# Kernel optimization log

Measured on AMD Instinct MI355X. Metric: run time of the kernel, lower is better.

Reference implementation:

```python
import jax, jax.numpy as jnp
import numpy as np

N, E, H = 20000, 320000, 2
F_IN, D, D_OUT, NMID = 17, 64, 32, 18
SLOPE, EPS = 0.2, 1e-5


def _gat(x, Wl, bl, Wr, br, att, bias, src, dst, n, h, c):
    # PyG GATv2Conv, heads=h, concat=False (mean over heads)
    xl = (x @ Wl + bl).reshape(n, h, c)   # source transform
    xr = (x @ Wr + br).reshape(n, h, c)   # target transform
    e = jax.nn.leaky_relu(xl[src] + xr[dst], SLOPE)        # [E,h,c]
    logit = jnp.sum(e * att, axis=-1)                       # [E,h]
    m = jax.ops.segment_max(logit, dst, num_segments=n)    # per-dst softmax
    a = jnp.exp(logit - m[dst])
    s = jax.ops.segment_sum(a, dst, num_segments=n)
    alpha = a / s[dst]
    out = jax.ops.segment_sum(alpha[..., None] * xl[src], dst, num_segments=n)
    return out.mean(axis=1) + bias


def _bn(x, g, b):
    # BatchNorm1d in training mode (batch statistics, biased variance)
    mu = x.mean(axis=0)
    var = jnp.mean((x - mu) ** 2, axis=0)
    return g * (x - mu) * jax.lax.rsqrt(var + EPS) + b


def setup_inputs() -> dict:
    key = jax.random.key(0)
    ks = iter(jax.random.split(key, 64))
    r = lambda *s: jax.random.normal(next(ks), s, jnp.float32) * 0.1
    return dict(
        x=jax.random.normal(next(ks), (N, F_IN), jnp.float32),
        src=jax.random.randint(next(ks), (E,), 0, N),
        dst=jax.random.randint(next(ks), (E,), 0, N),
        W0l=r(F_IN, H * D), b0l=r(H * D), W0r=r(F_IN, H * D), b0r=r(H * D),
        att0=r(H, D), bias0=r(D), g0=jnp.ones((D,), jnp.float32), be0=jnp.zeros((D,), jnp.float32),
        Wml=r(NMID, D, H * D), bml=r(NMID, H * D), Wmr=r(NMID, D, H * D), bmr=r(NMID, H * D),
        attm=r(NMID, H, D), biasm=r(NMID, D), gm=jnp.ones((NMID, D), jnp.float32), bem=jnp.zeros((NMID, D), jnp.float32),
        WLl=r(D, H * D_OUT), bLl=r(H * D_OUT), WLr=r(D, H * D_OUT), bLr=r(H * D_OUT),
        attL=r(H, D_OUT), biasL=r(D_OUT), gL=jnp.ones((D_OUT,), jnp.float32), beL=jnp.zeros((D_OUT,), jnp.float32),
        Wimp=r(D_OUT, 1), bimp=r(1), Wpol=r(D_OUT, 1), bpol=r(1),
    )


def reference(x, src, dst, W0l, b0l, W0r, b0r, att0, bias0, g0, be0,
              Wml, bml, Wmr, bmr, attm, biasm, gm, bem,
              WLl, bLl, WLr, bLr, attL, biasL, gL, beL,
              Wimp, bimp, Wpol, bpol):
    n = x.shape[0]
    loop = jnp.arange(n, dtype=src.dtype)  # add_self_loops=True (PyG default)
    s = jnp.concatenate([src, loop])
    d = jnp.concatenate([dst, loop])
    h = jax.nn.relu(_bn(_gat(x, W0l, b0l, W0r, b0r, att0, bias0, s, d, n, H, D), g0, be0))
    for i in range(NMID):
        h = h + jax.nn.relu(_bn(_gat(h, Wml[i], bml[i], Wmr[i], bmr[i], attm[i], biasm[i], s, d, n, H, D), gm[i], bem[i]))
    h = jax.nn.relu(_bn(_gat(h, WLl, bLl, WLr, bLr, attL, biasL, s, d, n, H, D_OUT), gL, beL))
    return (h @ Wimp + bimp, jax.nn.sigmoid(h @ Wpol + bpol))
```

## Files before the change

### kernel.cpp

```cpp
#include <hip/hip_runtime.h>
#include <hip/hip_fp16.h>
#include <math.h>

#define NN 20000
#define NE 320000
#define ET (NE + NN)
#define FIN 17
#define DD 64
#define DOUTC 32
#define NMIDL 18
#define SLOPE 0.2f
#define BN_EPS 1e-5f

typedef unsigned short ushortT;
typedef unsigned int uintT;

__device__ inline ushortT f2h(float x) { return __half_as_ushort(__float2half(x)); }
__device__ inline float2 h2unpack(uintT u) {
    __half2 h2 = *(__half2*)&u;
    return __half22float2(h2);
}


__global__ void k_init(int* __restrict__ deg, float* __restrict__ part) {
    int i = blockIdx.x * blockDim.x + threadIdx.x;
    if (i < NN) deg[i] = 1;
    if (i < 2 * 64 * 128) part[i] = 0.f;
}

__global__ void k_hist(const int* __restrict__ dst, int* __restrict__ deg) {
    int i = blockIdx.x * blockDim.x + threadIdx.x;
    if (i < NE) atomicAdd(&deg[dst[i]], 1);
}

__global__ __launch_bounds__(1024) void k_scan(const int* __restrict__ deg,
                                               int* __restrict__ row_ptr,
                                               int* __restrict__ cursor) {
    __shared__ int sarr[1024];
    int t = threadIdx.x;
    const int CH = 20;
    int base = t * CH;
    int sum = 0;
    for (int j = 0; j < CH; ++j) {
        int idx = base + j;
        if (idx < NN) sum += deg[idx];
    }
    sarr[t] = sum;
    __syncthreads();
    for (int off = 1; off < 1024; off <<= 1) {
        int v = (t >= off) ? sarr[t - off] : 0;
        __syncthreads();
        sarr[t] += v;
        __syncthreads();
    }
    int run = sarr[t] - sum;
    for (int j = 0; j < CH; ++j) {
        int idx = base + j;
        if (idx < NN) {
            row_ptr[idx] = run;
            cursor[idx] = run;
            run += deg[idx];
        }
    }
    if (t == 0) row_ptr[NN] = ET;
}

__global__ void k_scatter(const int* __restrict__ src, const int* __restrict__ dst,
                          int* __restrict__ cursor, int* __restrict__ edge_src) {
    int i = blockIdx.x * blockDim.x + threadIdx.x;
    if (i < NE) {
        int d = dst[i];
        int pos = atomicAdd(&cursor[d], 1);
        edge_src[pos] = src[i];
    } else if (i < ET) {
        int v = i - NE;
        int pos = atomicAdd(&cursor[v], 1);
        edge_src[pos] = v;
    }
}


template<int DIN, int DCOLS>
__global__ __launch_bounds__(256) void k_gemm3(const float* __restrict__ hin,
                                               const float* __restrict__ Wl, const float* __restrict__ bl,
                                               const float* __restrict__ Wr, const float* __restrict__ br,
                                               ushortT* __restrict__ xl, ushortT* __restrict__ xr) {
    constexpr int CG = (2 * DCOLS) / 64;
    constexpr int NSETS = 4 / CG;
    constexpr int NPB = NSETS * 4;
    int wave = __builtin_amdgcn_readfirstlane(threadIdx.x >> 6);
    int lane = threadIdx.x & 63;
    int cg = wave % CG;
    int nset = wave / CG;
    int col = cg * 64 + lane;
    bool isl = col < DCOLS;
    const float* W = isl ? Wl : Wr;
    ushortT* xo = isl ? xl : xr;
    int cw = col & (DCOLS - 1);
    float wreg[DIN];
    #pragma unroll
    for (int k = 0; k < DIN; ++k) wreg[k] = W[k * DCOLS + cw];
    float bias = (isl ? bl : br)[cw];

    for (int n0 = blockIdx.x * NPB + nset * 4; n0 < NN; n0 += gridDim.x * NPB) {
        const float* h0 = hin + (size_t)n0 * DIN;
        float a0 = 0.f, a1 = 0.f, a2 = 0.f, a3 = 0.f;
        #pragma unroll
        for (int k = 0; k < DIN; ++k) {
            float wk = wreg[k];
            a0 = fmaf(h0[k],           wk, a0);
            a1 = fmaf(h0[DIN + k],     wk, a1);
            a2 = fmaf(h0[2 * DIN + k], wk, a2);
            a3 = fmaf(h0[3 * DIN + k], wk, a3);
        }
        xo[(size_t)(n0 + 0) * DCOLS + cw] = f2h(a0 + bias);
        xo[(size_t)(n0 + 1) * DCOLS + cw] = f2h(a1 + bias);
        xo[(size_t)(n0 + 2) * DCOLS + cw] = f2h(a2 + bias);
        xo[(size_t)(n0 + 3) * DCOLS + cw] = f2h(a3 + bias);
    }
}


template<int DCOLS>
__global__ __launch_bounds__(256) void k_gemm_fused(
        const float* __restrict__ g, const float* __restrict__ part,
        float* __restrict__ partZero,
        const float* __restrict__ gam, const float* __restrict__ bet,
        int addres, float* __restrict__ hbuf,
        const float* __restrict__ Wl, const float* __restrict__ bl,
        const float* __restrict__ Wr, const float* __restrict__ br,
        ushortT* __restrict__ xl, ushortT* __restrict__ xr) {
    constexpr int DIN = 64;
    constexpr int CG = (2 * DCOLS) / 64;
    constexpr int NSETS = 4 / CG;
    constexpr int NPB = NSETS * 4;
    __shared__ float sscale[64], sshift[64];
    __shared__ float hlds[NPB][64];
    int tid = threadIdx.x;

    if (blockIdx.x == 0) {
        for (int i = tid; i < 64 * 128; i += 256) partZero[i] = 0.f;
    }
    {
        int c = tid & 63, half = tid >> 6;
        if (half < 2) {
            float ssum = 0.f;
            for (int s = 0; s < 64; ++s) ssum += part[s * 128 + half * 64 + c];
            hlds[half][c] = ssum;
        }
    }
    __syncthreads();
    if (tid < 64) {
        float mu  = hlds[0][tid] * (1.f / NN);
        float var = hlds[1][tid] * (1.f / NN) - mu * mu;
        float sc  = gam[tid] * rsqrtf(var + BN_EPS);
        sscale[tid] = sc;
        sshift[tid] = bet[tid] - sc * mu;
    }

    int wave = __builtin_amdgcn_readfirstlane(tid >> 6);
    int lane = tid & 63;
    int cg = wave % CG;
    int nset = wave / CG;
    int col = cg * 64 + lane;
    bool isl = col < DCOLS;
    const float* W = isl ? Wl : Wr;
    ushortT* xo = isl ? xl : xr;
    int cw = col & (DCOLS - 1);
    float wreg[DIN];
    #pragma unroll
    for (int k = 0; k < DIN; ++k) wreg[k] = W[k * DCOLS + cw];
    float bias = (isl ? bl : br)[cw];

    for (int n0 = blockIdx.x * NPB; n0 < NN; n0 += gridDim.x * NPB) {
        __syncthreads();
        #pragma unroll
        for (int v = 0; v < (NPB * 64) / 256; ++v) {
            int idx = tid + v * 256;
            int nl = idx >> 6, c = idx & 63;
            int node = n0 + nl;
            float gv = g[(size_t)node * 64 + c];
            float hv = fmaxf(fmaf(sscale[c], gv, sshift[c]), 0.f);
            if (addres) hv += hbuf[(size_t)node * 64 + c];
            hlds[nl][c] = hv;
            hbuf[(size_t)node * 64 + c] = hv;
        }
        __syncthreads();
        int nb = nset * 4;
        float a0 = 0.f, a1 = 0.f, a2 = 0.f, a3 = 0.f;
        #pragma unroll
        for (int k4 = 0; k4 < 16; ++k4) {
            float4 h0 = *(const float4*)&hlds[nb + 0][k4 * 4];
            float4 h1 = *(const float4*)&hlds[nb + 1][k4 * 4];
            float4 h2 = *(const float4*)&hlds[nb + 2][k4 * 4];
            float4 h3 = *(const float4*)&hlds[nb + 3][k4 * 4];
            a0 = fmaf(h0.x, wreg[k4*4+0], a0); a0 = fmaf(h0.y, wreg[k4*4+1], a0);
            a0 = fmaf(h0.z, wreg[k4*4+2], a0); a0 = fmaf(h0.w, wreg[k4*4+3], a0);
            a1 = fmaf(h1.x, wreg[k4*4+0], a1); a1 = fmaf(h1.y, wreg[k4*4+1], a1);
            a1 = fmaf(h1.z, wreg[k4*4+2], a1); a1 = fmaf(h1.w, wreg[k4*4+3], a1);
            a2 = fmaf(h2.x, wreg[k4*4+0], a2); a2 = fmaf(h2.y, wreg[k4*4+1], a2);
            a2 = fmaf(h2.z, wreg[k4*4+2], a2); a2 = fmaf(h2.w, wreg[k4*4+3], a2);
            a3 = fmaf(h3.x, wreg[k4*4+0], a3); a3 = fmaf(h3.y, wreg[k4*4+1], a3);
            a3 = fmaf(h3.z, wreg[k4*4+2], a3); a3 = fmaf(h3.w, wreg[k4*4+3], a3);
        }
        int nbase = n0 + nb;
        xo[(size_t)(nbase + 0) * DCOLS + cw] = f2h(a0 + bias);
        xo[(size_t)(nbase + 1) * DCOLS + cw] = f2h(a1 + bias);
        xo[(size_t)(nbase + 2) * DCOLS + cw] = f2h(a2 + bias);
        xo[(size_t)(nbase + 3) * DCOLS + cw] = f2h(a3 + bias);
    }
}


template<int CPL>
__global__ __launch_bounds__(256) void k_edge_stat(const ushortT* __restrict__ xl,
                                                   const ushortT* __restrict__ xr,
                                                   const float* __restrict__ att,
                                                   const float* __restrict__ bias,
                                                   const int* __restrict__ row_ptr,
                                                   const int* __restrict__ edge_src,
                                                   float* __restrict__ g,
                                                   float* __restrict__ partial) {
    constexpr int HC = CPL * 32;
    constexpr int RS = 2 * HC;
    int lane = threadIdx.x & 63;
    int node = blockIdx.x * 4 + (threadIdx.x >> 6);
    if (node >= NN) return;
    int co = lane * CPL;
    float2 xrv, attc;
    if (CPL == 2) {
        uintT ur = ((const uintT*)xr)[(size_t)node * (RS / 2) + lane];
        xrv = h2unpack(ur);
        attc = *(const float2*)&att[co];
    } else {
        xrv.x = __half2float(__ushort_as_half(xr[(size_t)node * RS + co]));
        xrv.y = 0.f;
        attc.x = att[co];
        attc.y = 0.f;
    }
    int beg = row_ptr[node], end = row_ptr[node + 1];
    float m = -1e30f, s = 0.f;
    float2 o = {0.f, 0.f};

    for (int cb = beg; cb < end; cb += 64) {
        int idx = cb + lane;
        int eload = edge_src[idx < end ? idx : end - 1];
        int cnt = min(64, end - cb);
        for (int b = 0; b < cnt; b += 8) {
            int nb = min(8, cnt - b);
            float p[8]; float2 xv[8];
            #pragma unroll
            for (int j = 0; j < 8; ++j) {
                int u = __shfl(eload, b + (j < nb ? j : 0));
                float2 v;
                if (CPL == 2) {
                    uintT uu = ((const uintT*)xl)[(size_t)u * (RS / 2) + lane];
                    v = h2unpack(uu);
                } else {
                    v.x = __half2float(__ushort_as_half(xl[(size_t)u * RS + co]));
                    v.y = 0.f;
                }
                xv[j] = v;
                float tx = v.x + xrv.x, ty = v.y + xrv.y;
                tx = tx > 0.f ? tx : SLOPE * tx;
                ty = ty > 0.f ? ty : SLOPE * ty;
                float pp = tx * attc.x + ty * attc.y;
                #pragma unroll
                for (int msk = 16; msk; msk >>= 1) pp += __shfl_xor(pp, msk);
                p[j] = (j < nb) ? pp : -1e30f;
            }
            float nm = fmaxf(fmaxf(fmaxf(p[0], p[1]), fmaxf(p[2], p[3])),
                             fmaxf(fmaxf(p[4], p[5]), fmaxf(p[6], p[7])));
            if (nm > m + 8.f) {
                float sc = __expf(m - nm);
                s *= sc; o.x *= sc; o.y *= sc;
                m = nm;
            }
            float w0 = __expf(p[0] - m), w1 = __expf(p[1] - m);
            float w2 = __expf(p[2] - m), w3 = __expf(p[3] - m);
            float w4 = __expf(p[4] - m), w5 = __expf(p[5] - m);
            float w6 = __expf(p[6] - m), w7 = __expf(p[7] - m);
            s += ((w0 + w1) + (w2 + w3)) + ((w4 + w5) + (w6 + w7));
            o.x += ((w0 * xv[0].x + w1 * xv[1].x) + (w2 * xv[2].x + w3 * xv[3].x))
                 + ((w4 * xv[4].x + w5 * xv[5].x) + (w6 * xv[6].x + w7 * xv[7].x));
            o.y += ((w0 * xv[0].y + w1 * xv[1].y) + (w2 * xv[2].y + w3 * xv[3].y))
                 + ((w4 * xv[4].y + w5 * xv[5].y) + (w6 * xv[6].y + w7 * xv[7].y));
        }
    }
    float inv = 1.f / s;
    float rx = o.x * inv, ry = o.y * inv;
    float ox = __shfl_xor(rx, 32);
    float oy = __shfl_xor(ry, 32);
    if (lane < 32) {
        float* ps = &partial[(size_t)(node & 63) * 128];
        if (CPL == 2) {
            float2 bv = *(const float2*)&bias[co];
            float2 outv = { 0.5f * (rx + ox) + bv.x, 0.5f * (ry + oy) + bv.y };
            *(float2*)&g[(size_t)node * HC + co] = outv;
            atomicAdd(&ps[co],     outv.x);
            atomicAdd(&ps[co + 1], outv.y);
            atomicAdd(&ps[64 + co],     outv.x * outv.x);
            atomicAdd(&ps[64 + co + 1], outv.y * outv.y);
        } else {
            float ov = 0.5f * (rx + ox) + bias[co];
            g[(size_t)node * HC + co] = ov;
            atomicAdd(&ps[co], ov);
            atomicAdd(&ps[64 + co], ov * ov);
        }
    }
}


__global__ __launch_bounds__(256) void k_headf(const float* __restrict__ g,
                                               const float* __restrict__ part,
                                               const float* __restrict__ gL, const float* __restrict__ beL,
                                               const float* __restrict__ Wimp, const float* __restrict__ bimp,
                                               const float* __restrict__ Wpol, const float* __restrict__ bpol,
                                               float* __restrict__ out) {
    __shared__ float tmp[2][32];
    __shared__ float sscale[32], sshift[32], swi[32], swp[32];
    int tid = threadIdx.x;
    if (tid < 64) {
        int c = tid & 31, half = tid >> 5;
        float ssum = 0.f;
        for (int s = 0; s < 64; ++s) ssum += part[s * 128 + half * 64 + c];
        tmp[half][c] = ssum;
    }
    __syncthreads();
    if (tid < 32) {
        float mu  = tmp[0][tid] * (1.f / NN);
        float var = tmp[1][tid] * (1.f / NN) - mu * mu;
        float sc  = gL[tid] * rsqrtf(var + BN_EPS);
        sscale[tid] = sc;
        sshift[tid] = beL[tid] - sc * mu;
        swi[tid] = Wimp[tid];
        swp[tid] = Wpol[tid];
    }
    __syncthreads();
    int n = blockIdx.x * 256 + tid;
    if (n >= NN) return;
    float a1 = bimp[0], a2 = bpol[0];
    #pragma unroll
    for (int k = 0; k < DOUTC; ++k) {
        float hv = fmaxf(fmaf(sscale[k], g[(size_t)n * DOUTC + k], sshift[k]), 0.f);
        a1 = fmaf(hv, swi[k], a1);
        a2 = fmaf(hv, swp[k], a2);
    }
    out[n] = a1;
    out[NN + n] = 1.f / (1.f + expf(-a2));
}


extern "C" void kernel_launch(void* const* d_in, const int* in_sizes, int n_in,
                              void* d_out, int out_size, void* d_ws, size_t ws_size,
                              hipStream_t stream) {
    const float* x    = (const float*)d_in[0];
    const int*   src  = (const int*)d_in[1];
    const int*   dst  = (const int*)d_in[2];
    const float* W0l  = (const float*)d_in[3];
    const float* b0l  = (const float*)d_in[4];
    const float* W0r  = (const float*)d_in[5];
    const float* b0r  = (const float*)d_in[6];
    const float* att0 = (const float*)d_in[7];
    const float* bias0= (const float*)d_in[8];
    const float* g0   = (const float*)d_in[9];
    const float* be0  = (const float*)d_in[10];
    const float* Wml  = (const float*)d_in[11];
    const float* bml  = (const float*)d_in[12];
    const float* Wmr  = (const float*)d_in[13];
    const float* bmr  = (const float*)d_in[14];
    const float* attm = (const float*)d_in[15];
    const float* biasm= (const float*)d_in[16];
    const float* gm   = (const float*)d_in[17];
    const float* bem  = (const float*)d_in[18];
    const float* WLl  = (const float*)d_in[19];
    const float* bLl  = (const float*)d_in[20];
    const float* WLr  = (const float*)d_in[21];
    const float* bLr  = (const float*)d_in[22];
    const float* attL = (const float*)d_in[23];
    const float* biasL= (const float*)d_in[24];
    const float* gL   = (const float*)d_in[25];
    const float* beL  = (const float*)d_in[26];
    const float* Wimp = (const float*)d_in[27];
    const float* bimp = (const float*)d_in[28];
    const float* Wpol = (const float*)d_in[29];
    const float* bpol = (const float*)d_in[30];
    float* out = (float*)d_out;

    char* w = (char*)d_ws;
    size_t off = 0;
    auto alloc = [&](size_t bytes) -> char* {
        char* p = w + off;
        off += (bytes + 511) & ~(size_t)511;
        return p;
    };
    int* deg      = (int*)alloc(NN * 4);
    int* cursor   = (int*)alloc(NN * 4);
    int* row_ptr  = (int*)alloc((NN + 1) * 4);
    int* edge_src = (int*)alloc(ET * 4);
    ushortT* xl = (ushortT*)alloc((size_t)NN * 128 * 2);
    ushortT* xr = (ushortT*)alloc((size_t)NN * 128 * 2);
    float* gbuf = (float*)alloc((size_t)NN * 64 * 4);
    float* hbuf = (float*)alloc((size_t)NN * 64 * 4);
    float* part = (float*)alloc(2 * 64 * 128 * 4);
    float* part0 = part;
    float* part1 = part + 64 * 128;

    k_init<<<(NN + 255) / 256, 256, 0, stream>>>(deg, part);
    k_hist<<<(NE + 255) / 256, 256, 0, stream>>>(dst, deg);
    k_scan<<<1, 1024, 0, stream>>>(deg, row_ptr, cursor);
    k_scatter<<<(ET + 255) / 256, 256, 0, stream>>>(src, dst, cursor, edge_src);

    k_gemm3<FIN, 128><<<1250, 256, 0, stream>>>(x, W0l, b0l, W0r, b0r, xl, xr);
    k_edge_stat<2><<<(NN + 3) / 4, 256, 0, stream>>>(xl, xr, att0, bias0, row_ptr, edge_src, gbuf, part0);

    for (int L = 1; L <= NMIDL; ++L) {
        int i = L - 1;
        const float* pg = (L == 1) ? g0  : gm  + (size_t)(L - 2) * DD;
        const float* pb = (L == 1) ? be0 : bem + (size_t)(L - 2) * DD;
        float* pPrev = (L & 1) ? part0 : part1;
        float* pNext = (L & 1) ? part1 : part0;
        k_gemm_fused<128><<<1250, 256, 0, stream>>>(
            gbuf, pPrev, pNext, pg, pb, (L >= 2) ? 1 : 0, hbuf,
            Wml + (size_t)i * DD * 128, bml + (size_t)i * 128,
            Wmr + (size_t)i * DD * 128, bmr + (size_t)i * 128, xl, xr);
        k_edge_stat<2><<<(NN + 3) / 4, 256, 0, stream>>>(xl, xr, attm + (size_t)i * 128,
                                                         biasm + (size_t)i * DD, row_ptr, edge_src, gbuf, pNext);
    }

    {
        int L = 19;
        const float* pg = gm  + (size_t)(L - 2) * DD;
        const float* pb = bem + (size_t)(L - 2) * DD;
        float* pPrev = part0;
        float* pNext = part1;
        k_gemm_fused<64><<<1250, 256, 0, stream>>>(
            gbuf, pPrev, pNext, pg, pb, 1, hbuf,
            WLl, bLl, WLr, bLr, xl, xr);
        k_edge_stat<1><<<(NN + 3) / 4, 256, 0, stream>>>(xl, xr, attL, biasL, row_ptr, edge_src, gbuf, pNext);
    }

    k_headf<<<(NN + 255) / 256, 256, 0, stream>>>(gbuf, part1, gL, beL, Wimp, bimp, Wpol, bpol, out);
}
```

Baseline: 1.274 ms.

## Split wavefront halves across edges with wider per-lane feature loads in edge softmax

The edge aggregation kernel now has each half-wavefront handle a different group of 8 edges, so 16 edges are processed per iteration. Each lane loads 2 or 4 contiguous fp16 channels covering both heads, the reduction shuffle width shrinks to 16 lanes, and the two halves' online-softmax states are merged at the end with a max-rescale. This raises memory-level parallelism per gather and halves the shuffle-reduction work per edge. The cost is more registers per lane and an extra merge step, and padded slots are masked to zero weight.

```diff
diff --git a/kernel.cpp b/kernel.cpp
--- a/kernel.cpp
+++ b/kernel.cpp
@@ -212,7 +212,7 @@
 }
 
 
-template<int CPL>
+template<int UPL>
 __global__ __launch_bounds__(256) void k_edge_stat(const ushortT* __restrict__ xl,
                                                    const ushortT* __restrict__ xr,
                                                    const float* __restrict__ att,
@@ -221,91 +221,117 @@
                                                    const int* __restrict__ edge_src,
                                                    float* __restrict__ g,
                                                    float* __restrict__ partial) {
-    constexpr int HC = CPL * 32;
-    constexpr int RS = 2 * HC;
+    constexpr int HC = 32 * UPL;
+    constexpr int UROW = HC;
+    constexpr int CK = 2 * UPL;
     int lane = threadIdx.x & 63;
     int node = blockIdx.x * 4 + (threadIdx.x >> 6);
     if (node >= NN) return;
-    int co = lane * CPL;
-    float2 xrv, attc;
-    if (CPL == 2) {
-        uintT ur = ((const uintT*)xr)[(size_t)node * (RS / 2) + lane];
-        xrv = h2unpack(ur);
-        attc = *(const float2*)&att[co];
-    } else {
-        xrv.x = __half2float(__ushort_as_half(xr[(size_t)node * RS + co]));
-        xrv.y = 0.f;
-        attc.x = att[co];
-        attc.y = 0.f;
-    }
+    int half = lane >> 5;
+    int hl = lane & 31;
+    int d0 = CK * hl;
+
+    float xrv[CK], attc[CK];
+    const uintT* xru = (const uintT*)xr;
+    #pragma unroll
+    for (int q = 0; q < UPL; ++q) {
+        float2 v = h2unpack(xru[(size_t)node * UROW + UPL * hl + q]);
+        xrv[2*q]   = v.x; xrv[2*q+1]   = v.y;
+        attc[2*q]  = att[d0 + 2*q];
+        attc[2*q+1]= att[d0 + 2*q + 1];
+    }
+    const uintT* xlu = (const uintT*)xl;
     int beg = row_ptr[node], end = row_ptr[node + 1];
     float m = -1e30f, s = 0.f;
-    float2 o = {0.f, 0.f};
+    float o[CK];
+    #pragma unroll
+    for (int k = 0; k < CK; ++k) o[k] = 0.f;
 
     for (int cb = beg; cb < end; cb += 64) {
         int idx = cb + lane;
         int eload = edge_src[idx < end ? idx : end - 1];
         int cnt = min(64, end - cb);
-        for (int b = 0; b < cnt; b += 8) {
-            int nb = min(8, cnt - b);
-            float p[8]; float2 xv[8];
+        for (int b = 0; b < cnt; b += 16) {
+            float p[8];
+            float xv[8][CK];
             #pragma unroll
             for (int j = 0; j < 8; ++j) {
-                int u = __shfl(eload, b + (j < nb ? j : 0));
-                float2 v;
-                if (CPL == 2) {
-                    uintT uu = ((const uintT*)xl)[(size_t)u * (RS / 2) + lane];
-                    v = h2unpack(uu);
+                int slot = b + 8 * half + j;
+                int u = __shfl(eload, slot);
+                if (UPL == 2) {
+                    uint2 dw = *(const uint2*)(xlu + (size_t)u * UROW + 2 * hl);
+                    float2 va = h2unpack(dw.x), vb = h2unpack(dw.y);
+                    xv[j][0] = va.x; xv[j][1] = va.y;
+                    xv[j][2] = vb.x; xv[j][3] = vb.y;
                 } else {
-                    v.x = __half2float(__ushort_as_half(xl[(size_t)u * RS + co]));
-                    v.y = 0.f;
+                    float2 va = h2unpack(xlu[(size_t)u * UROW + hl]);
+                    xv[j][0] = va.x; xv[j][1] = va.y;
                 }
-                xv[j] = v;
-                float tx = v.x + xrv.x, ty = v.y + xrv.y;
-                tx = tx > 0.f ? tx : SLOPE * tx;
-                ty = ty > 0.f ? ty : SLOPE * ty;
-                float pp = tx * attc.x + ty * attc.y;
+                float pp = 0.f;
                 #pragma unroll
-                for (int msk = 16; msk; msk >>= 1) pp += __shfl_xor(pp, msk);
-                p[j] = (j < nb) ? pp : -1e30f;
+                for (int k = 0; k < CK; ++k) {
+                    float t = xv[j][k] + xrv[k];
+                    t = fmaxf(t, t * SLOPE);
+                    pp = fmaf(t, attc[k], pp);
+                }
+                #pragma unroll
+                for (int msk = 8; msk; msk >>= 1) pp += __shfl_xor(pp, msk);
+                p[j] = (slot < cnt) ? pp : -1e30f;
             }
             float nm = fmaxf(fmaxf(fmaxf(p[0], p[1]), fmaxf(p[2], p[3])),
                              fmaxf(fmaxf(p[4], p[5]), fmaxf(p[6], p[7])));
             if (nm > m + 8.f) {
                 float sc = __expf(m - nm);
-                s *= sc; o.x *= sc; o.y *= sc;
+                s *= sc;
+                #pragma unroll
+                for (int k = 0; k < CK; ++k) o[k] *= sc;
                 m = nm;
             }
-            float w0 = __expf(p[0] - m), w1 = __expf(p[1] - m);
-            float w2 = __expf(p[2] - m), w3 = __expf(p[3] - m);
-            float w4 = __expf(p[4] - m), w5 = __expf(p[5] - m);
-            float w6 = __expf(p[6] - m), w7 = __expf(p[7] - m);
-            s += ((w0 + w1) + (w2 + w3)) + ((w4 + w5) + (w6 + w7));
-            o.x += ((w0 * xv[0].x + w1 * xv[1].x) + (w2 * xv[2].x + w3 * xv[3].x))
-                 + ((w4 * xv[4].x + w5 * xv[5].x) + (w6 * xv[6].x + w7 * xv[7].x));
-            o.y += ((w0 * xv[0].y + w1 * xv[1].y) + (w2 * xv[2].y + w3 * xv[3].y))
-                 + ((w4 * xv[4].y + w5 * xv[5].y) + (w6 * xv[6].y + w7 * xv[7].y));
+            #pragma unroll
+            for (int j = 0; j < 8; ++j) {
+                float w = (p[j] > -1e29f) ? __expf(p[j] - m) : 0.f;
+                s += w;
+                #pragma unroll
+                for (int k = 0; k < CK; ++k) o[k] = fmaf(w, xv[j][k], o[k]);
+            }
+        }
+    }
+
+    {
+        float mo = __shfl_xor(m, 32);
+        float so = __shfl_xor(s, 32);
+        float mm = fmaxf(m, mo);
+        float ea = __expf(m - mm), eb = __expf(mo - mm);
+        s = s * ea + so * eb;
+        #pragma unroll
+        for (int k = 0; k < CK; ++k) {
+            float ok = __shfl_xor(o[k], 32);
+            o[k] = o[k] * ea + ok * eb;
         }
     }
     float inv = 1.f / s;
-    float rx = o.x * inv, ry = o.y * inv;
-    float ox = __shfl_xor(rx, 32);
-    float oy = __shfl_xor(ry, 32);
-    if (lane < 32) {
+    float r[CK], rh[CK];
+    #pragma unroll
+    for (int k = 0; k < CK; ++k) {
+        r[k] = o[k] * inv;
+        rh[k] = __shfl_xor(r[k], 16);
+    }
+    if (lane < 16) {
+        float outv[CK];
+        #pragma unroll
+        for (int k = 0; k < CK; ++k) outv[k] = 0.5f * (r[k] + rh[k]) + bias[d0 + k];
+        if (UPL == 2) {
+            float4 o4 = { outv[0], outv[1], outv[2], outv[3] };
+            *(float4*)&g[(size_t)node * HC + d0] = o4;
+        } else {
+            float2 o2 = { outv[0], outv[1] };
+            *(float2*)&g[(size_t)node * HC + d0] = o2;
+        }
         float* ps = &partial[(size_t)(node & 63) * 128];
-        if (CPL == 2) {
-            float2 bv = *(const float2*)&bias[co];
-            float2 outv = { 0.5f * (rx + ox) + bv.x, 0.5f * (ry + oy) + bv.y };
-            *(float2*)&g[(size_t)node * HC + co] = outv;
-            atomicAdd(&ps[co],     outv.x);
-            atomicAdd(&ps[co + 1], outv.y);
-            atomicAdd(&ps[64 + co],     outv.x * outv.x);
-            atomicAdd(&ps[64 + co + 1], outv.y * outv.y);
-        } else {
-            float ov = 0.5f * (rx + ox) + bias[co];
-            g[(size_t)node * HC + co] = ov;
-            atomicAdd(&ps[co], ov);
-            atomicAdd(&ps[64 + co], ov * ov);
+        #pragma unroll
+        for (int k = 0; k < CK; ++k) {
+            atomicAdd(&ps[d0 + k], outv[k]);
+            atomicAdd(&ps[64 + d0 + k], outv[k] * outv[k]);
         }
     }
 }
```

Result: slower. 1.456 ms (+14.3%).
